# Performance work log

Measured on AMD Instinct MI355X. Metric: run time of the kernel, lower is better.

## Reference

```python
import jax, jax.numpy as jnp
import numpy as np

N_NODES = 100000
N_EDGES = 1_600_000
IN_C, HID_C, CLS_C = 128, 256, 64


def setup_inputs() -> dict:
    key = jax.random.key(0)
    ks = jax.random.split(key, 8)
    x = jax.random.normal(ks[0], (N_NODES, IN_C), dtype=jnp.float32)
    edge_index = jax.random.randint(ks[1], (2, N_EDGES), 0, N_NODES, dtype=jnp.int64)
    s1 = 1.0 / np.sqrt(IN_C)
    s2 = 1.0 / np.sqrt(HID_C)
    W1l = jax.random.uniform(ks[2], (IN_C, HID_C), jnp.float32, -s1, s1)
    W1r = jax.random.uniform(ks[3], (IN_C, HID_C), jnp.float32, -s1, s1)
    b1 = jnp.zeros((HID_C,), jnp.float32)
    W2l = jax.random.uniform(ks[4], (HID_C, CLS_C), jnp.float32, -s2, s2)
    W2r = jax.random.uniform(ks[5], (HID_C, CLS_C), jnp.float32, -s2, s2)
    b2 = jnp.zeros((CLS_C,), jnp.float32)
    return {"x": x, "edge_index": edge_index,
            "W1l": W1l, "W1r": W1r, "b1": b1,
            "W2l": W2l, "W2r": W2r, "b2": b2}


def _sage_conv(x, src, dst, Wl, Wr, b, num_nodes):
    # mean aggregation of source features onto destination nodes
    agg = jax.ops.segment_sum(x[src], dst, num_segments=num_nodes)  # [N, F]
    deg = jax.ops.segment_sum(jnp.ones((src.shape[0], 1), x.dtype), dst,
                              num_segments=num_nodes)               # [N, 1]
    agg = agg / jnp.maximum(deg, 1.0)  # zero-degree nodes -> 0
    return agg @ Wl + x @ Wr + b


def reference(x, edge_index, W1l, W1r, b1, W2l, W2r, b2):
    src, dst = edge_index[0], edge_index[1]
    n = x.shape[0]
    h = jax.nn.relu(_sage_conv(x, src, dst, W1l, W1r, b1, n))
    # dropout(p=0.5) is identity in eval mode
    out = _sage_conv(h, src, dst, W2l, W2r, b2, n)
    return jax.nn.sigmoid(out)
```

## Files before the change

### kernel.cpp

```cpp
#include <hip/hip_runtime.h>

typedef __attribute__((ext_vector_type(8))) short short8;
typedef __attribute__((ext_vector_type(4))) float floatx4;
typedef __attribute__((ext_vector_type(2))) float floatx2;

static __device__ __forceinline__ unsigned short f2bf(float f) {
  unsigned int u = __builtin_bit_cast(unsigned int, f);
  u += 0x7FFFu + ((u >> 16) & 1u);
  return (unsigned short)(u >> 16);
}
static __device__ __forceinline__ float bf2f(unsigned short s) {
  unsigned int u = ((unsigned int)s) << 16;
  return __builtin_bit_cast(float, u);
}
static __device__ __forceinline__ unsigned int pk4_fp8(float a, float b, float c, float d) {
  int lo = __builtin_amdgcn_cvt_pk_fp8_f32(a, b, 0, false);
  int hi = __builtin_amdgcn_cvt_pk_fp8_f32(c, d, 0, false);
  return (unsigned int)((lo & 0xffff) | ((hi & 0xffff) << 16));
}
static __device__ __forceinline__ floatx4 unpk4_fp8(unsigned int p) {
  floatx2 lo = __builtin_amdgcn_cvt_pk_f32_fp8((int)p, false);
  floatx2 hi = __builtin_amdgcn_cvt_pk_f32_fp8((int)p, true);
  floatx4 r = {lo.x, lo.y, hi.x, hi.y};
  return r;
}

#define NBUCK 2048
#define BIN_CHUNK 8192
#define SCAP 1536

__global__ __launch_bounds__(256) void binscatter(const int* __restrict__ src,
                                                  const int* __restrict__ dst,
                                                  int* __restrict__ bcnt,
                                                  unsigned int* __restrict__ staging,
                                                  int E) {
  __shared__ int h[NBUCK];
  __shared__ int cur[NBUCK];
  for (int i = threadIdx.x; i < NBUCK; i += 256) h[i] = 0;
  __syncthreads();
  int base = blockIdx.x * BIN_CHUNK;
  int end = base + BIN_CHUNK; if (end > E) end = E;
  for (int i = base + threadIdx.x; i < end; i += 256)
    atomicAdd(&h[dst[i] >> 6], 1);
  __syncthreads();
  for (int i = threadIdx.x; i < NBUCK; i += 256)
    cur[i] = h[i] ? atomicAdd(&bcnt[i], h[i]) : 0;
  __syncthreads();
  for (int i = base + threadIdx.x; i < end; i += 256) {
    int d = dst[i], s = src[i];
    int b = d >> 6;
    int pos = atomicAdd(&cur[b], 1);
    if (pos < SCAP)
      staging[(size_t)b * SCAP + pos] = ((unsigned int)(d & 63) << 17) | (unsigned int)s;
  }
}

__global__ void convw(const float* __restrict__ W1l, const float* __restrict__ W1r,
                      const float* __restrict__ W2l, const float* __restrict__ W2r,
                      unsigned short* __restrict__ W1p, unsigned short* __restrict__ W2p) {
  int i = blockIdx.x * blockDim.x + threadIdx.x;
  if (i < 8192) {
    int lane = i & 63, ni = (i >> 6) & 1, kk = (i >> 7) & 7, w = i >> 10;
    int fm = lane & 15, fq = lane >> 4;
    int n = w * 32 + ni * 16 + fm;
    int k0 = kk * 32 + fq * 8;
    unsigned short r[8];
#pragma unroll
    for (int j = 0; j < 8; j++) {
      int k = k0 + j;
      float v = (k < 128) ? W1l[k * 256 + n] : W1r[(k - 128) * 256 + n];
      r[j] = f2bf(v);
    }
    *reinterpret_cast<uint4*>(W1p + (size_t)i * 8) = *reinterpret_cast<uint4*>(r);
  } else if (i < 8192 + 4096) {
    int j2 = i - 8192;
    int lane = j2 & 63, kk = (j2 >> 6) & 7, w = j2 >> 9;
    int fm = lane & 15, fq = lane >> 4;
    int n = w * 16 + fm;
    int k0 = kk * 32 + fq * 8;
    unsigned short r[8];
#pragma unroll
    for (int j = 0; j < 8; j++) {
      int k = k0 + j;
      float v = (n < 64) ? W2l[k * 64 + n] : W2r[k * 64 + (n - 64)];
      r[j] = f2bf(v);
    }
    *reinterpret_cast<uint4*>(W2p + (size_t)j2 * 8) = *reinterpret_cast<uint4*>(r);
  }
}

__global__ void convx(const float* __restrict__ x, unsigned int* __restrict__ xq,
                      unsigned short* __restrict__ xbf, int n_nodes) {
  int i = blockIdx.x * blockDim.x + threadIdx.x;
  if (i < n_nodes * 32) {
    int node = i >> 5, c4 = (i & 31) * 4;
    float4 v = *reinterpret_cast<const float4*>(x + (size_t)node * 128 + c4);
    xq[i] = pk4_fp8(v.x, v.y, v.z, v.w);
    unsigned short r[4] = { f2bf(v.x), f2bf(v.y), f2bf(v.z), f2bf(v.w) };
    *reinterpret_cast<uint2*>(xbf + (size_t)node * 128 + c4) =
        *reinterpret_cast<uint2*>(r);
  }
}

#define LDSW 264
__global__ __launch_bounds__(512, 6) void gemm_fused(const unsigned short* __restrict__ xbf,
                                                     const uint4* __restrict__ xq,
                                                     const unsigned int* __restrict__ staging,
                                                     const int* __restrict__ bcnt,
                                                     const unsigned short* __restrict__ W1p,
                                                     const unsigned short* __restrict__ W2p,
                                                     const float* __restrict__ b1,
                                                     unsigned char* __restrict__ zq,
                                                     unsigned short* __restrict__ rb,
                                                     int* __restrict__ csr_src,
                                                     int* __restrict__ rs,
                                                     int* __restrict__ deg,
                                                     int M) {
  __shared__ unsigned short smem[64 * LDSW];
  __shared__ int eidx[SCAP];
  __shared__ int h64[64], rstart[64], cur64[64];
  const int tid = threadIdx.x;
  const int lane = tid & 63;
  const int wave = tid >> 6;
  const int m0 = blockIdx.x * 64;
  const int fm = lane & 15;
  const int fq = lane >> 4;
  const int base = blockIdx.x * SCAP;
  int cnt = bcnt[blockIdx.x]; if (cnt > SCAP) cnt = SCAP;
  const short8* __restrict__ W1v = reinterpret_cast<const short8*>(W1p);
  const short8* __restrict__ W2v = reinterpret_cast<const short8*>(W2p);

  if (tid < 64) h64[tid] = 0;
  __syncthreads();

#pragma unroll
  for (int j = 0; j < 2; j++) {
    int c = j * 512 + tid;
    int row = c >> 4, u4 = c & 15;
    int gr = m0 + row; if (gr >= M) gr = M - 1;
    uint4 v = *reinterpret_cast<const uint4*>(xbf + (size_t)gr * 128 + u4 * 8);
    *reinterpret_cast<uint4*>(&smem[row * LDSW + 128 + u4 * 8]) = v;
  }

  for (int i = tid; i < cnt; i += 512)
    atomicAdd(&h64[staging[base + i] >> 17], 1);
  __syncthreads();

  if (tid < 64) {
    int v = h64[tid];
    int s = v;
#pragma unroll
    for (int off = 1; off < 64; off <<= 1) {
      int o = __shfl_up(s, off, 64);
      if (tid >= off) s += o;
    }
    int excl = s - v;
    rstart[tid] = excl;
    cur64[tid] = excl;
    int w = m0 + tid;
    if (w < M) { rs[w] = base + excl; deg[w] = v; }
  }
  __syncthreads();

  for (int i = tid; i < cnt; i += 512) {
    unsigned int wv = staging[base + i];
    int pos = atomicAdd(&cur64[wv >> 17], 1);
    if (pos < SCAP) eidx[pos] = (int)(wv & 0x1FFFFu);
  }
  __syncthreads();

  for (int i = tid; i < cnt; i += 512)
    csr_src[base + i] = eidx[i];

  {
    const int grp = lane >> 3;
    const int ch4 = lane & 7;
    int row = wave * 8 + grp;
    int e0l = rstart[row];
    int e1l = e0l + h64[row];
    if (e1l > SCAP) e1l = SCAP;
    floatx4 a0[4] = {{0,0,0,0},{0,0,0,0},{0,0,0,0},{0,0,0,0}};
    floatx4 a1[4] = {{0,0,0,0},{0,0,0,0},{0,0,0,0},{0,0,0,0}};
    for (int e = e0l; e < e1l; e += 8) {
      uint4 pb[8];
#pragma unroll
      for (int j = 0; j < 8; j++) {
        int t = e + j; if (t >= e1l) t = e1l - 1;
        int s = eidx[t];
        pb[j] = xq[(s << 3) | ch4];
      }
      int rem = e1l - e;
#pragma unroll
      for (int j = 0; j < 8; j++) {
        if (j < rem) {
          floatx4* acc = (j & 1) ? a1 : a0;
          acc[0] += unpk4_fp8(pb[j].x);
          acc[1] += unpk4_fp8(pb[j].y);
          acc[2] += unpk4_fp8(pb[j].z);
          acc[3] += unpk4_fp8(pb[j].w);
        }
      }
    }
    int d = e1l - e0l; if (d < 1) d = 1;
    float sc = 1.0f / (float)d;
    unsigned short r[16];
#pragma unroll
    for (int j = 0; j < 4; j++) {
      floatx4 a = a0[j] + a1[j];
      r[4 * j + 0] = f2bf(a.x * sc); r[4 * j + 1] = f2bf(a.y * sc);
      r[4 * j + 2] = f2bf(a.z * sc); r[4 * j + 3] = f2bf(a.w * sc);
    }
    unsigned short* dstp = &smem[row * LDSW + ch4 * 16];
    *reinterpret_cast<uint4*>(dstp) = *reinterpret_cast<uint4*>(r);
    *reinterpret_cast<uint4*>(dstp + 8) = *reinterpret_cast<uint4*>(r + 8);
  }

  float bb[2];
#pragma unroll
  for (int ni = 0; ni < 2; ni++) bb[ni] = b1[wave * 32 + ni * 16 + fm];

  __syncthreads();

  floatx4 acc1[4][2] = {};
#pragma unroll 2
  for (int kk = 0; kk < 8; kk++) {
    short8 af[4], bfr[2];
#pragma unroll
    for (int mi = 0; mi < 4; mi++)
      af[mi] = *reinterpret_cast<const short8*>(
          &smem[(mi * 16 + fm) * LDSW + kk * 32 + fq * 8]);
#pragma unroll
    for (int ni = 0; ni < 2; ni++)
      bfr[ni] = W1v[((wave * 8 + kk) * 2 + ni) * 64 + lane];
#pragma unroll
    for (int mi = 0; mi < 4; mi++)
#pragma unroll
      for (int ni = 0; ni < 2; ni++)
        acc1[mi][ni] = __builtin_amdgcn_mfma_f32_16x16x32_bf16(af[mi], bfr[ni],
                                                               acc1[mi][ni], 0, 0, 0);
  }

  __syncthreads();

#pragma unroll
  for (int mi = 0; mi < 4; mi++)
#pragma unroll
    for (int ni = 0; ni < 2; ni++)
#pragma unroll
      for (int r = 0; r < 4; r++) {
        float v = acc1[mi][ni][r] + bb[ni];
        v = v > 0.f ? v : 0.f;
        smem[(mi * 16 + fq * 4 + r) * LDSW + wave * 32 + ni * 16 + fm] = f2bf(v);
      }
  __syncthreads();

  floatx4 acc2[4] = {};
#pragma unroll 2
  for (int kk = 0; kk < 8; kk++) {
    short8 hf[4];
#pragma unroll
    for (int mi = 0; mi < 4; mi++)
      hf[mi] = *reinterpret_cast<const short8*>(
          &smem[(mi * 16 + fm) * LDSW + kk * 32 + fq * 8]);
    short8 wf = W2v[(wave * 8 + kk) * 64 + lane];
#pragma unroll
    for (int mi = 0; mi < 4; mi++)
      acc2[mi] = __builtin_amdgcn_mfma_f32_16x16x32_bf16(hf[mi], wf, acc2[mi], 0, 0, 0);
  }

#pragma unroll
  for (int mi = 0; mi < 4; mi++)
#pragma unroll
    for (int r = 0; r < 4; r++) {
      int grow = m0 + mi * 16 + fq * 4 + r;
      if (grow < M) {
        float v = acc2[mi][r];
        if (wave < 4) {
          int col = wave * 16 + fm;
          int b8 = __builtin_amdgcn_cvt_pk_fp8_f32(v, v, 0, false);
          zq[grow * 64 + col] = (unsigned char)(b8 & 0xff);
        } else {
          int col = (wave - 4) * 16 + fm;
          rb[grow * 64 + col] = f2bf(v);
        }
      }
    }
}

__global__ __launch_bounds__(256) void agg2_final(const uint4* __restrict__ zq,
                                                  const unsigned short* __restrict__ rb,
                                                  const int* __restrict__ csr_src,
                                                  const int* __restrict__ rs,
                                                  const int* __restrict__ deg,
                                                  const float* __restrict__ b2,
                                                  float* __restrict__ out, int n_nodes) {
  int lane = threadIdx.x & 63;
  int wave = threadIdx.x >> 6;
  int grp = lane >> 2;
  int ch = lane & 3;
  int lbase = lane & 60;
  int w = blockIdx.x * 64 + wave * 16 + grp;
  if (w >= n_nodes) return;
  int e0 = rs[w], e1 = e0 + deg[w];
  floatx4 a0[4] = {{0,0,0,0},{0,0,0,0},{0,0,0,0},{0,0,0,0}};
  floatx4 a1[4] = {{0,0,0,0},{0,0,0,0},{0,0,0,0},{0,0,0,0}};
  for (int e = e0; e < e1; e += 8) {
    int tA = e + ch;     if (tA >= e1) tA = e1 - 1;
    int tB = e + 4 + ch; if (tB >= e1) tB = e1 - 1;
    int iA = csr_src[tA];
    int iB = csr_src[tB];
    uint4 pb[8];
#pragma unroll
    for (int j = 0; j < 4; j++) {
      int s = __shfl(iA, lbase | j, 64);
      pb[j] = zq[(s << 2) | ch];
    }
#pragma unroll
    for (int j = 0; j < 4; j++) {
      int s = __shfl(iB, lbase | j, 64);
      pb[4 + j] = zq[(s << 2) | ch];
    }
    int rem = e1 - e;
#pragma unroll
    for (int j = 0; j < 8; j++) {
      if (j < rem) {
        floatx4* acc = (j & 1) ? a1 : a0;
        acc[0] += unpk4_fp8(pb[j].x);
        acc[1] += unpk4_fp8(pb[j].y);
        acc[2] += unpk4_fp8(pb[j].z);
        acc[3] += unpk4_fp8(pb[j].w);
      }
    }
  }
  int d = e1 - e0; if (d < 1) d = 1;
  float sc = 1.0f / (float)d;
  const unsigned short* rbp = rb + w * 64 + ch * 16;
  const float* b2p = b2 + ch * 16;
  float* op = out + (size_t)w * 64 + ch * 16;
#pragma unroll
  for (int j = 0; j < 4; j++) {
    floatx4 a = a0[j] + a1[j];
    uint2 rr = *reinterpret_cast<const uint2*>(rbp + 4 * j);
    float4 bv = *reinterpret_cast<const float4*>(b2p + 4 * j);
    float r0 = bf2f((unsigned short)(rr.x & 0xffff));
    float r1 = bf2f((unsigned short)(rr.x >> 16));
    float r2 = bf2f((unsigned short)(rr.y & 0xffff));
    float r3 = bf2f((unsigned short)(rr.y >> 16));
    float4 o;
    o.x = 1.0f / (1.0f + __expf(-(a.x * sc + r0 + bv.x)));
    o.y = 1.0f / (1.0f + __expf(-(a.y * sc + r1 + bv.y)));
    o.z = 1.0f / (1.0f + __expf(-(a.z * sc + r2 + bv.z)));
    o.w = 1.0f / (1.0f + __expf(-(a.w * sc + r3 + bv.w)));
    *reinterpret_cast<float4*>(op + 4 * j) = o;
  }
}

extern "C" void kernel_launch(void* const* d_in, const int* in_sizes, int n_in,
                              void* d_out, int out_size, void* d_ws, size_t ws_size,
                              hipStream_t stream) {
  const float* x   = (const float*)d_in[0];
  const int*   ei  = (const int*)d_in[1];
  const float* W1l = (const float*)d_in[2];
  const float* W1r = (const float*)d_in[3];
  const float* b1  = (const float*)d_in[4];
  const float* W2l = (const float*)d_in[5];
  const float* W2r = (const float*)d_in[6];
  const float* b2  = (const float*)d_in[7];
  float* out = (float*)d_out;

  const int N = in_sizes[0] / 128;
  const int E = in_sizes[1] / 2;
  const int* src = ei;
  const int* dst = ei + E;

  char* wsb = (char*)d_ws;
  size_t off = 0;
  auto alloc = [&](size_t bytes) -> void* {
    void* p = wsb + off;
    off += (bytes + 511) & ~(size_t)511;
    return p;
  };
  int* rs       = (int*)alloc((size_t)N * 4);
  int* deg      = (int*)alloc((size_t)N * 4);
  int* bcnt     = (int*)alloc(NBUCK * 4);
  int* csr_src  = (int*)alloc((size_t)NBUCK * SCAP * 4);
  unsigned int* staging = (unsigned int*)alloc((size_t)NBUCK * SCAP * 4);
  unsigned short* W1p = (unsigned short*)alloc(256 * 256 * 2);
  unsigned short* W2p = (unsigned short*)alloc(128 * 256 * 2);
  unsigned int* xq    = (unsigned int*)alloc((size_t)N * 128);
  unsigned short* xbf = (unsigned short*)alloc((size_t)N * 128 * 2);
  unsigned char* zq   = (unsigned char*)alloc((size_t)N * 64);
  unsigned short* rb  = (unsigned short*)alloc((size_t)N * 64 * 2);
  (void)ws_size; (void)n_in; (void)out_size;

  const int ntiles = (N + 63) / 64;
  const int nchunks = (E + BIN_CHUNK - 1) / BIN_CHUNK;

  hipMemsetAsync(bcnt, 0, NBUCK * 4, stream);
  binscatter<<<nchunks, 256, 0, stream>>>(src, dst, bcnt, staging, E);

  convw<<<(8192 + 4096 + 255) / 256, 256, 0, stream>>>(W1l, W1r, W2l, W2r, W1p, W2p);
  convx<<<(N * 32 + 255) / 256, 256, 0, stream>>>(x, xq, xbf, N);

  gemm_fused<<<ntiles, 512, 0, stream>>>(xbf, (const uint4*)xq, staging, bcnt,
                                         W1p, W2p, b1, zq, rb, csr_src, rs, deg, N);

  agg2_final<<<(N + 63) / 64, 256, 0, stream>>>((const uint4*)zq, rb, csr_src, rs, deg,
                                                b2, out, N);
}
```

Before: 235.6 us.

## Rebuild per-tile CSR in LDS in agg2 instead of writing global csr arrays

The gemm kernel no longer writes csr_src, rs and deg to global memory. agg2_final now reloads the staging bucket per 64-node tile, rebuilds the local CSR in LDS with a histogram, scan and scatter, then gathers fp8 rows at 8 lanes per node using uint2 loads. Staging entries are held in registers (three per thread) instead of being reloaded for each pass. This removes global CSR write and read traffic, but duplicates the bucket sort work in the second kernel. It also assumes cnt is at most 1536 and drops the SCAP clamp on e1l.

Result: faster. 229.0 us (-2.8%).

```diff
diff --git a/kernel.cpp b/kernel.cpp
--- a/kernel.cpp
+++ b/kernel.cpp
@@ -112,9 +112,6 @@
                                                      const float* __restrict__ b1,
                                                      unsigned char* __restrict__ zq,
                                                      unsigned short* __restrict__ rb,
-                                                     int* __restrict__ csr_src,
-                                                     int* __restrict__ rs,
-                                                     int* __restrict__ deg,
                                                      int M) {
   __shared__ unsigned short smem[64 * LDSW];
   __shared__ int eidx[SCAP];
@@ -133,6 +130,12 @@
   if (tid < 64) h64[tid] = 0;
   __syncthreads();
 
+  unsigned int ew0 = 0, ew1 = 0, ew2 = 0;
+  const int i0 = tid, i1 = tid + 512, i2 = tid + 1024;
+  if (i0 < cnt) ew0 = staging[base + i0];
+  if (i1 < cnt) ew1 = staging[base + i1];
+  if (i2 < cnt) ew2 = staging[base + i2];
+
 #pragma unroll
   for (int j = 0; j < 2; j++) {
     int c = j * 512 + tid;
@@ -142,8 +145,9 @@
     *reinterpret_cast<uint4*>(&smem[row * LDSW + 128 + u4 * 8]) = v;
   }
 
-  for (int i = tid; i < cnt; i += 512)
-    atomicAdd(&h64[staging[base + i] >> 17], 1);
+  if (i0 < cnt) atomicAdd(&h64[ew0 >> 17], 1);
+  if (i1 < cnt) atomicAdd(&h64[ew1 >> 17], 1);
+  if (i2 < cnt) atomicAdd(&h64[ew2 >> 17], 1);
   __syncthreads();
 
   if (tid < 64) {
@@ -157,20 +161,13 @@
     int excl = s - v;
     rstart[tid] = excl;
     cur64[tid] = excl;
-    int w = m0 + tid;
-    if (w < M) { rs[w] = base + excl; deg[w] = v; }
-  }
-  __syncthreads();
-
-  for (int i = tid; i < cnt; i += 512) {
-    unsigned int wv = staging[base + i];
-    int pos = atomicAdd(&cur64[wv >> 17], 1);
-    if (pos < SCAP) eidx[pos] = (int)(wv & 0x1FFFFu);
-  }
-  __syncthreads();
-
-  for (int i = tid; i < cnt; i += 512)
-    csr_src[base + i] = eidx[i];
+  }
+  __syncthreads();
+
+  if (i0 < cnt) { int p = atomicAdd(&cur64[ew0 >> 17], 1); eidx[p] = (int)(ew0 & 0x1FFFFu); }
+  if (i1 < cnt) { int p = atomicAdd(&cur64[ew1 >> 17], 1); eidx[p] = (int)(ew1 & 0x1FFFFu); }
+  if (i2 < cnt) { int p = atomicAdd(&cur64[ew2 >> 17], 1); eidx[p] = (int)(ew2 & 0x1FFFFu); }
+  __syncthreads();
 
   {
     const int grp = lane >> 3;
@@ -178,7 +175,6 @@
     int row = wave * 8 + grp;
     int e0l = rstart[row];
     int e1l = e0l + h64[row];
-    if (e1l > SCAP) e1l = SCAP;
     floatx4 a0[4] = {{0,0,0,0},{0,0,0,0},{0,0,0,0},{0,0,0,0}};
     floatx4 a1[4] = {{0,0,0,0},{0,0,0,0},{0,0,0,0},{0,0,0,0}};
     for (int e = e0l; e < e1l; e += 8) {
@@ -287,72 +283,99 @@
     }
 }
 
-__global__ __launch_bounds__(256) void agg2_final(const uint4* __restrict__ zq,
-                                                  const unsigned short* __restrict__ rb,
-                                                  const int* __restrict__ csr_src,
-                                                  const int* __restrict__ rs,
-                                                  const int* __restrict__ deg,
-                                                  const float* __restrict__ b2,
-                                                  float* __restrict__ out, int n_nodes) {
-  int lane = threadIdx.x & 63;
-  int wave = threadIdx.x >> 6;
-  int grp = lane >> 2;
-  int ch = lane & 3;
-  int lbase = lane & 60;
-  int w = blockIdx.x * 64 + wave * 16 + grp;
+__global__ __launch_bounds__(512, 6) void agg2_final(const uint2* __restrict__ zq2,
+                                                     const unsigned short* __restrict__ rb,
+                                                     const unsigned int* __restrict__ staging,
+                                                     const int* __restrict__ bcnt,
+                                                     const float* __restrict__ b2,
+                                                     float* __restrict__ out, int n_nodes) {
+  __shared__ int eidx[SCAP];
+  __shared__ int h64[64], rstart[64], cur64[64];
+  const int tid = threadIdx.x;
+  const int lane = tid & 63;
+  const int wave = tid >> 6;
+  const int m0 = blockIdx.x * 64;
+  const int base = blockIdx.x * SCAP;
+  int cnt = bcnt[blockIdx.x]; if (cnt > SCAP) cnt = SCAP;
+
+  if (tid < 64) h64[tid] = 0;
+  __syncthreads();
+
+  unsigned int ew0 = 0, ew1 = 0, ew2 = 0;
+  const int i0 = tid, i1 = tid + 512, i2 = tid + 1024;
+  if (i0 < cnt) ew0 = staging[base + i0];
+  if (i1 < cnt) ew1 = staging[base + i1];
+  if (i2 < cnt) ew2 = staging[base + i2];
+  if (i0 < cnt) atomicAdd(&h64[ew0 >> 17], 1);
+  if (i1 < cnt) atomicAdd(&h64[ew1 >> 17], 1);
+  if (i2 < cnt) atomicAdd(&h64[ew2 >> 17], 1);
+  __syncthreads();
+
+  if (tid < 64) {
+    int v = h64[tid];
+    int s = v;
+#pragma unroll
+    for (int off = 1; off < 64; off <<= 1) {
+      int o = __shfl_up(s, off, 64);
+      if (tid >= off) s += o;
+    }
+    rstart[tid] = s - v;
+    cur64[tid] = s - v;
+  }
+  __syncthreads();
+
+  if (i0 < cnt) { int p = atomicAdd(&cur64[ew0 >> 17], 1); eidx[p] = (int)(ew0 & 0x1FFFFu); }
+  if (i1 < cnt) { int p = atomicAdd(&cur64[ew1 >> 17], 1); eidx[p] = (int)(ew1 & 0x1FFFFu); }
+  if (i2 < cnt) { int p = atomicAdd(&cur64[ew2 >> 17], 1); eidx[p] = (int)(ew2 & 0x1FFFFu); }
+  __syncthreads();
+
+  const int grp = lane >> 3;
+  const int ch = lane & 7;
+  int row = wave * 8 + grp;
+  int w = m0 + row;
   if (w >= n_nodes) return;
-  int e0 = rs[w], e1 = e0 + deg[w];
-  floatx4 a0[4] = {{0,0,0,0},{0,0,0,0},{0,0,0,0},{0,0,0,0}};
-  floatx4 a1[4] = {{0,0,0,0},{0,0,0,0},{0,0,0,0},{0,0,0,0}};
-  for (int e = e0; e < e1; e += 8) {
-    int tA = e + ch;     if (tA >= e1) tA = e1 - 1;
-    int tB = e + 4 + ch; if (tB >= e1) tB = e1 - 1;
-    int iA = csr_src[tA];
-    int iB = csr_src[tB];
-    uint4 pb[8];
-#pragma unroll
-    for (int j = 0; j < 4; j++) {
-      int s = __shfl(iA, lbase | j, 64);
-      pb[j] = zq[(s << 2) | ch];
-    }
-#pragma unroll
-    for (int j = 0; j < 4; j++) {
-      int s = __shfl(iB, lbase | j, 64);
-      pb[4 + j] = zq[(s << 2) | ch];
-    }
-    int rem = e1 - e;
+  int e0l = rstart[row];
+  int e1l = e0l + h64[row];
+  floatx4 a0[2] = {{0,0,0,0},{0,0,0,0}};
+  floatx4 a1[2] = {{0,0,0,0},{0,0,0,0}};
+  for (int e = e0l; e < e1l; e += 8) {
+    uint2 pb[8];
+#pragma unroll
+    for (int j = 0; j < 8; j++) {
+      int t = e + j; if (t >= e1l) t = e1l - 1;
+      int s = eidx[t];
+      pb[j] = zq2[(s << 3) | ch];
+    }
+    int rem = e1l - e;
 #pragma unroll
     for (int j = 0; j < 8; j++) {
       if (j < rem) {
         floatx4* acc = (j & 1) ? a1 : a0;
         acc[0] += unpk4_fp8(pb[j].x);
         acc[1] += unpk4_fp8(pb[j].y);
-        acc[2] += unpk4_fp8(pb[j].z);
-        acc[3] += unpk4_fp8(pb[j].w);
       }
     }
   }
-  int d = e1 - e0; if (d < 1) d = 1;
+  int d = e1l - e0l; if (d < 1) d = 1;
   float sc = 1.0f / (float)d;
-  const unsigned short* rbp = rb + w * 64 + ch * 16;
-  const float* b2p = b2 + ch * 16;
-  float* op = out + (size_t)w * 64 + ch * 16;
-#pragma unroll
-  for (int j = 0; j < 4; j++) {
-    floatx4 a = a0[j] + a1[j];
-    uint2 rr = *reinterpret_cast<const uint2*>(rbp + 4 * j);
-    float4 bv = *reinterpret_cast<const float4*>(b2p + 4 * j);
-    float r0 = bf2f((unsigned short)(rr.x & 0xffff));
-    float r1 = bf2f((unsigned short)(rr.x >> 16));
-    float r2 = bf2f((unsigned short)(rr.y & 0xffff));
-    float r3 = bf2f((unsigned short)(rr.y >> 16));
-    float4 o;
-    o.x = 1.0f / (1.0f + __expf(-(a.x * sc + r0 + bv.x)));
-    o.y = 1.0f / (1.0f + __expf(-(a.y * sc + r1 + bv.y)));
-    o.z = 1.0f / (1.0f + __expf(-(a.z * sc + r2 + bv.z)));
-    o.w = 1.0f / (1.0f + __expf(-(a.w * sc + r3 + bv.w)));
-    *reinterpret_cast<float4*>(op + 4 * j) = o;
-  }
+  int c0 = ch * 8;
+  uint4 rr = *reinterpret_cast<const uint4*>(rb + (size_t)w * 64 + c0);
+  float4 bvA = *reinterpret_cast<const float4*>(b2 + c0);
+  float4 bvB = *reinterpret_cast<const float4*>(b2 + c0 + 4);
+  floatx4 s0 = a0[0] + a1[0];
+  floatx4 s1 = a0[1] + a1[1];
+  float4 oA, oB;
+  oA.x = 1.0f / (1.0f + __expf(-(s0.x * sc + bf2f((unsigned short)(rr.x & 0xffff)) + bvA.x)));
+  oA.y = 1.0f / (1.0f + __expf(-(s0.y * sc + bf2f((unsigned short)(rr.x >> 16)) + bvA.y)));
+  oA.z = 1.0f / (1.0f + __expf(-(s0.z * sc + bf2f((unsigned short)(rr.y & 0xffff)) + bvA.z)));
+  oA.w = 1.0f / (1.0f + __expf(-(s0.w * sc + bf2f((unsigned short)(rr.y >> 16)) + bvA.w)));
+  oB.x = 1.0f / (1.0f + __expf(-(s1.x * sc + bf2f((unsigned short)(rr.z & 0xffff)) + bvB.x)));
+  oB.y = 1.0f / (1.0f + __expf(-(s1.y * sc + bf2f((unsigned short)(rr.z >> 16)) + bvB.y)));
+  oB.z = 1.0f / (1.0f + __expf(-(s1.z * sc + bf2f((unsigned short)(rr.w & 0xffff)) + bvB.z)));
+  oB.w = 1.0f / (1.0f + __expf(-(s1.w * sc + bf2f((unsigned short)(rr.w >> 16)) + bvB.w)));
+  float* op = out + (size_t)w * 64 + c0;
+  *reinterpret_cast<float4*>(op) = oA;
+  *reinterpret_cast<float4*>(op + 4) = oB;
 }
 
 extern "C" void kernel_launch(void* const* d_in, const int* in_sizes, int n_in,
@@ -380,10 +403,7 @@
     off += (bytes + 511) & ~(size_t)511;
     return p;
   };
-  int* rs       = (int*)alloc((size_t)N * 4);
-  int* deg      = (int*)alloc((size_t)N * 4);
   int* bcnt     = (int*)alloc(NBUCK * 4);
-  int* csr_src  = (int*)alloc((size_t)NBUCK * SCAP * 4);
   unsigned int* staging = (unsigned int*)alloc((size_t)NBUCK * SCAP * 4);
   unsigned short* W1p = (unsigned short*)alloc(256 * 256 * 2);
   unsigned short* W2p = (unsigned short*)alloc(128 * 256 * 2);
@@ -403,8 +423,8 @@
   convx<<<(N * 32 + 255) / 256, 256, 0, stream>>>(x, xq, xbf, N);
 
   gemm_fused<<<ntiles, 512, 0, stream>>>(xbf, (const uint4*)xq, staging, bcnt,
-                                         W1p, W2p, b1, zq, rb, csr_src, rs, deg, N);
-
-  agg2_final<<<(N + 63) / 64, 256, 0, stream>>>((const uint4*)zq, rb, csr_src, rs, deg,
-                                                b2, out, N);
-}
+                                         W1p, W2p, b1, zq, rb, N);
+
+  agg2_final<<<ntiles, 512, 0, stream>>>((const uint2*)zq, rb, staging, bcnt,
+                                         b2, out, N);
+}
```
